# Optimization experiments

Hardware: AMD Instinct MI355X
Metric: run time of the kernel (lower is better)

Reference implementation:

```python
import jax, jax.numpy as jnp
import numpy as np


def _gcn(x, src, dst, W, b, n):
    # symmetric normalization: deg computed on edges WITH self-loops (weights 1)
    deg = jax.ops.segment_sum(jnp.ones_like(src, dtype=x.dtype), dst, num_segments=n)
    dinv = jnp.where(deg > 0, jax.lax.rsqrt(deg), 0.0)
    norm = dinv[src] * dinv[dst]              # [E+n]
    xw = x @ W                                # [n, out] transform first (cheaper)
    msg = xw[src] * norm[:, None]             # gather + edge scale
    return jax.ops.segment_sum(msg, dst, num_segments=n) + b


def setup_inputs() -> dict:
    key = jax.random.key(0)
    ks = jax.random.split(key, 8)
    N, E = 100_000, 1_280_000
    x = jax.random.normal(ks[0], (N, 18), dtype=jnp.float32)
    edge_index = jax.random.randint(ks[1], (2, E), 0, N, dtype=jnp.int32)
    W1 = jax.random.normal(ks[2], (18, 32), dtype=jnp.float32) * 0.2
    b1 = jnp.zeros((32,), dtype=jnp.float32)
    W2 = jax.random.normal(ks[3], (32, 64), dtype=jnp.float32) * 0.15
    b2 = jnp.zeros((64,), dtype=jnp.float32)
    Wfc = jax.random.normal(ks[4], (64, 2), dtype=jnp.float32) * 0.1
    bfc = jnp.zeros((2,), dtype=jnp.float32)
    return {"x": x, "edge_index": edge_index, "W1": W1, "b1": b1,
            "W2": W2, "b2": b2, "Wfc": Wfc, "bfc": bfc}


def reference(x, edge_index, W1, b1, W2, b2, Wfc, bfc):
    n = x.shape[0]
    loop = jnp.arange(n, dtype=edge_index.dtype)
    src = jnp.concatenate([edge_index[0], loop])   # add self-loops (PyG default)
    dst = jnp.concatenate([edge_index[1], loop])
    h = jax.nn.relu(_gcn(x, src, dst, W1, b1, n))
    h = jax.nn.relu(_gcn(h, src, dst, W2, b2, n))
    logits = h @ Wfc + bfc
    return jax.nn.log_softmax(logits, axis=1)
```

## Files before the change

kernel.cpp:

```cpp
#include <hip/hip_runtime.h>
#include <hip/hip_fp16.h>
#include <math.h>


#define TPB 256
#define BSH 8
#define BNODES 256
#define MAXBUCK 512
#define CH 4096
#define CAPSH 13
#define CAP (1 << CAPSH)

__global__ void k_part(const int* __restrict__ src, const int* __restrict__ dst,
                       int* __restrict__ bcursor, int* __restrict__ eb,
                       __half* __restrict__ u1h, __half* __restrict__ u2h,
                       int E, int n, int nbuck) {
    __shared__ int lh[MAXBUCK];
    __shared__ int lexc[MAXBUCK];
    __shared__ int lbase[MAXBUCK];
    __shared__ int sval[CH];
    __shared__ unsigned short sbk[CH];
    int t = threadIdx.x;
    if (blockIdx.x == 0 && t < 32) {
        u1h[(size_t)n * 32 + t] = __float2half_rn(0.f);
        u2h[(size_t)n * 32 + t] = __float2half_rn(0.f);
    }
    int chunk0 = blockIdx.x * CH;
    int end = min(chunk0 + CH, E);
    int cnt = end - chunk0;
    const int4* dst4 = (const int4*)dst;
    const int4* src4 = (const int4*)src;
    for (int i = t; i < MAXBUCK; i += TPB) lh[i] = 0;
    __syncthreads();
    for (int e4 = chunk0 / 4 + t; e4 * 4 < end; e4 += TPB) {
        int base = e4 * 4;
        int4 d = dst4[e4];
        if (base + 0 < end) atomicAdd(&lh[d.x >> BSH], 1);
        if (base + 1 < end) atomicAdd(&lh[d.y >> BSH], 1);
        if (base + 2 < end) atomicAdd(&lh[d.z >> BSH], 1);
        if (base + 3 < end) atomicAdd(&lh[d.w >> BSH], 1);
    }
    __syncthreads();
    for (int i = t; i < MAXBUCK; i += TPB) lexc[i] = lh[i];
    __syncthreads();
    for (int off = 1; off < MAXBUCK; off <<= 1) {
        int i1 = t + TPB;
        int v0 = (t >= off) ? lexc[t - off] : 0;
        int v1 = (i1 >= off) ? lexc[i1 - off] : 0;
        __syncthreads();
        lexc[t] += v0;
        lexc[i1] += v1;
        __syncthreads();
    }
    for (int i = t; i < MAXBUCK; i += TPB) {
        int c = lh[i];
        lbase[i] = c ? atomicAdd(&bcursor[i], c) : 0;
        lexc[i] -= c;
        lh[i] = 0;
    }
    __syncthreads();
    for (int e4 = chunk0 / 4 + t; e4 * 4 < end; e4 += TPB) {
        int base = e4 * 4;
        int4 d = dst4[e4];
        int4 s = src4[e4];
        #define PUTL(c, sv) if (base + c < end) { \
            int b = (d.sv) >> BSH; \
            int p = lexc[b] + atomicAdd(&lh[b], 1); \
            sval[p] = ((s.sv) << BSH) | ((d.sv) & (BNODES - 1)); \
            sbk[p] = (unsigned short)b; }
        PUTL(0, x) PUTL(1, y) PUTL(2, z) PUTL(3, w)
        #undef PUTL
    }
    __syncthreads();
    for (int i = t; i < cnt; i += TPB) {
        int b = sbk[i];
        int r = lbase[b] + (i - lexc[b]);
        if (r < CAP) eb[((size_t)b << CAPSH) + r] = sval[i];
    }
}

__global__ void k_bucket(const int* __restrict__ eb, const int* __restrict__ bcursor,
                         const float* __restrict__ x, const float* __restrict__ W1,
                         int* __restrict__ csr, int* __restrict__ row_start,
                         int* __restrict__ cnt8, float* __restrict__ dinv,
                         __half* __restrict__ u1h, int n) {
    __shared__ int lcnt[BNODES];
    __shared__ int lscan[BNODES];
    __shared__ float ldinv[BNODES];
    __shared__ float xs[BNODES * 18];
    int b = blockIdx.x;
    int t = threadIdx.x;
    int node0 = b << BSH;
    int beg = b << CAPSH;
    int end = beg + min(bcursor[b], CAP);
    lcnt[t] = 0;
    __syncthreads();
    for (int i = beg + t; i < end; i += TPB)
        atomicAdd(&lcnt[eb[i] & (BNODES - 1)], 1);
    __syncthreads();
    int v = lcnt[t];
    int pad = (v + 7) & ~7;
    lscan[t] = pad;
    __syncthreads();
    for (int off = 1; off < TPB; off <<= 1) {
        int xx = (t >= off) ? lscan[t - off] : 0;
        __syncthreads();
        lscan[t] += xx;
        __syncthreads();
    }
    int pexcl = lscan[t] - pad;
    int node = node0 + t;
    float dv = rsqrtf(1.0f + (float)v);
    ldinv[t] = dv;
    if (node < n) {
        row_start[node] = beg + pexcl;
        cnt8[node] = pad >> 3;
        dinv[node] = dv;
    }
    __syncthreads();
    lcnt[t] = pexcl;
    __syncthreads();
    for (int i = beg + t; i < end; i += TPB) {
        int e = eb[i];
        int p = atomicAdd(&lcnt[e & (BNODES - 1)], 1);
        csr[beg + p] = e >> BSH;
    }
    __syncthreads();
    for (int p = v; p < pad; ++p) csr[beg + pexcl + p] = n;
    int nn = min(BNODES, n - node0);
    const float* xb = x + (size_t)node0 * 18;
    int tot18 = nn * 18;
    for (int i = t; i < tot18; i += TPB) xs[i] = xb[i];
    __syncthreads();
    int f = t & 31, g = t >> 5;
    float w1r[18];
#pragma unroll
    for (int k = 0; k < 18; ++k) w1r[k] = W1[k * 32 + f];
    __half* ub = u1h + (size_t)node0 * 32;
    for (int nl = g; nl < nn; nl += 8) {
        const float* rp = &xs[nl * 18];
        float a = 0.f;
#pragma unroll
        for (int k = 0; k < 18; ++k) a = fmaf(rp[k], w1r[k], a);
        ub[nl * 32 + f] = __float2half_rn(a * ldinv[nl]);
    }
}

#define CVT4(vv, r0, r1, r2, r3) \
    { __half2* _p = (__half2*)&(vv); \
      float2 _fl = __half22float2(_p[0]), _fh = __half22float2(_p[1]); \
      r0 = _fl.x; r1 = _fl.y; r2 = _fh.x; r3 = _fh.y; }

#define GATHER8H(uq, sA, sB, q, a0, a1, a2, a3) \
    { uint2 _v0 = uq[(size_t)(sA).x * 8 + (q)]; \
      uint2 _v1 = uq[(size_t)(sA).y * 8 + (q)]; \
      uint2 _v2 = uq[(size_t)(sA).z * 8 + (q)]; \
      uint2 _v3 = uq[(size_t)(sA).w * 8 + (q)]; \
      uint2 _v4 = uq[(size_t)(sB).x * 8 + (q)]; \
      uint2 _v5 = uq[(size_t)(sB).y * 8 + (q)]; \
      uint2 _v6 = uq[(size_t)(sB).z * 8 + (q)]; \
      uint2 _v7 = uq[(size_t)(sB).w * 8 + (q)]; \
      __half2* _h0 = (__half2*)&_v0; __half2* _h1 = (__half2*)&_v1; \
      __half2* _h2 = (__half2*)&_v2; __half2* _h3 = (__half2*)&_v3; \
      __half2* _h4 = (__half2*)&_v4; __half2* _h5 = (__half2*)&_v5; \
      __half2* _h6 = (__half2*)&_v6; __half2* _h7 = (__half2*)&_v7; \
      __half2 _A01 = __hadd2(_h0[0], _h1[0]), _A23 = __hadd2(_h2[0], _h3[0]); \
      __half2 _A45 = __hadd2(_h4[0], _h5[0]), _A67 = __hadd2(_h6[0], _h7[0]); \
      __half2 _B01 = __hadd2(_h0[1], _h1[1]), _B23 = __hadd2(_h2[1], _h3[1]); \
      __half2 _B45 = __hadd2(_h4[1], _h5[1]), _B67 = __hadd2(_h6[1], _h7[1]); \
      __half2 _A03 = __hadd2(_A01, _A23), _A47 = __hadd2(_A45, _A67); \
      __half2 _B03 = __hadd2(_B01, _B23), _B47 = __hadd2(_B45, _B67); \
      float2 _fa0 = __half22float2(_A03), _fa1 = __half22float2(_A47); \
      float2 _fb0 = __half22float2(_B03), _fb1 = __half22float2(_B47); \
      a0 += _fa0.x + _fa1.x; \
      a1 += _fa0.y + _fa1.y; \
      a2 += _fb0.x + _fb1.x; \
      a3 += _fb0.y + _fb1.y; }

__global__ void k_fused1(const uint2* __restrict__ u1q, const int* __restrict__ row_start,
                         const int* __restrict__ cnt8, const int* __restrict__ csr,
                         const float* __restrict__ dinv,
                         const float* __restrict__ b1, __half* __restrict__ u2h,
                         int n) {
    int t = threadIdx.x;
    int lane = t & 63, wv = t >> 6;
    int q = lane & 7, grp = lane >> 3;
    int node = (blockIdx.x * 4 + wv) * 8 + grp;
    if (node >= n) return;
    float4 bb = ((const float4*)b1)[q];
    uint2 sv = u1q[(size_t)node * 8 + q];
    float a0, a1, a2, a3;
    CVT4(sv, a0, a1, a2, a3)
    int beg = row_start[node];
    int it = cnt8[node];
    const int4* ip = (const int4*)(csr + beg);
    if (it > 0) {
        int4 sA = ip[0], sB = ip[1];
        for (int i = 0; i < it; ++i) {
            int4 nA = ip[2 * i + 2];
            int4 nB = ip[2 * i + 3];
            GATHER8H(u1q, sA, sB, q, a0, a1, a2, a3)
            sA = nA; sB = nB;
        }
    }
    float di = dinv[node];
    float r0 = fmaxf(fmaf(di, a0, bb.x), 0.f) * di;
    float r1 = fmaxf(fmaf(di, a1, bb.y), 0.f) * di;
    float r2 = fmaxf(fmaf(di, a2, bb.z), 0.f) * di;
    float r3 = fmaxf(fmaf(di, a3, bb.w), 0.f) * di;
    uint2 st;
    __half2* sp = (__half2*)&st;
    sp[0].x = __float2half_rn(r0); sp[0].y = __float2half_rn(r1);
    sp[1].x = __float2half_rn(r2); sp[1].y = __float2half_rn(r3);
    ((uint2*)u2h)[(size_t)node * 8 + q] = st;
}

__global__ void k_fused2(const uint2* __restrict__ u2q, const int* __restrict__ row_start,
                         const int* __restrict__ cnt8, const int* __restrict__ csr,
                         const float* __restrict__ dinv,
                         const float* __restrict__ W2,
                         const float* __restrict__ b2, const float* __restrict__ Wfc,
                         const float* __restrict__ bfc, float* __restrict__ out,
                         int n) {
    __shared__ float lagg[4][8][33];
    int t = threadIdx.x;
    int lane = t & 63, wv = t >> 6;
    int q = lane & 7, grp = lane >> 3;
    float w2r[32];
#pragma unroll
    for (int k = 0; k < 32; ++k) w2r[k] = W2[k * 64 + lane];
    float b2v = b2[lane];
    float wf0 = Wfc[lane * 2 + 0], wf1 = Wfc[lane * 2 + 1];
    float bf0 = bfc[0], bf1 = bfc[1];
    int node0 = (blockIdx.x * 4 + wv) * 8;
    int node = node0 + grp;
    float a0 = 0.f, a1 = 0.f, a2 = 0.f, a3 = 0.f;
    if (node < n) {
        uint2 sv = u2q[(size_t)node * 8 + q];
        float s0, s1, s2, s3;
        CVT4(sv, s0, s1, s2, s3)
        a0 = s0; a1 = s1; a2 = s2; a3 = s3;
        int beg = row_start[node];
        int it = cnt8[node];
        const int4* ip = (const int4*)(csr + beg);
        if (it > 0) {
            int4 sA = ip[0], sB = ip[1];
            for (int i = 0; i < it; ++i) {
                int4 nA = ip[2 * i + 2];
                int4 nB = ip[2 * i + 3];
                GATHER8H(u2q, sA, sB, q, a0, a1, a2, a3)
                sA = nA; sB = nB;
            }
        }
    }
    lagg[wv][grp][4 * q + 0] = a0;
    lagg[wv][grp][4 * q + 1] = a1;
    lagg[wv][grp][4 * q + 2] = a2;
    lagg[wv][grp][4 * q + 3] = a3;
#pragma unroll
    for (int r = 0; r < 8; ++r) {
        int nodeT = node0 + r;
        const float* rp = lagg[wv][r];
        float c0 = 0.f, c1 = 0.f, c2 = 0.f, c3 = 0.f;
#pragma unroll
        for (int k = 0; k < 32; k += 4) {
            c0 = fmaf(rp[k],     w2r[k],     c0);
            c1 = fmaf(rp[k + 1], w2r[k + 1], c1);
            c2 = fmaf(rp[k + 2], w2r[k + 2], c2);
            c3 = fmaf(rp[k + 3], w2r[k + 3], c3);
        }
        float a = (c0 + c1) + (c2 + c3);
        float v = (nodeT < n) ? fmaxf(fmaf(dinv[nodeT], a, b2v), 0.f) : 0.f;
        float l0 = v * wf0;
        float l1 = v * wf1;
#pragma unroll
        for (int off = 32; off >= 1; off >>= 1) {
            l0 += __shfl_xor(l0, off, 64);
            l1 += __shfl_xor(l1, off, 64);
        }
        if (lane == 0 && nodeT < n) {
            l0 += bf0;
            l1 += bf1;
            float m2 = fmaxf(l0, l1);
            float lse = m2 + logf(expf(l0 - m2) + expf(l1 - m2));
            out[nodeT * 2 + 0] = l0 - lse;
            out[nodeT * 2 + 1] = l1 - lse;
        }
    }
}

extern "C" void kernel_launch(void* const* d_in, const int* in_sizes, int n_in,
                              void* d_out, int out_size, void* d_ws, size_t ws_size,
                              hipStream_t stream) {
    const float* x   = (const float*)d_in[0];
    const int*   ei  = (const int*)d_in[1];
    const float* W1  = (const float*)d_in[2];
    const float* b1  = (const float*)d_in[3];
    const float* W2  = (const float*)d_in[4];
    const float* b2  = (const float*)d_in[5];
    const float* Wfc = (const float*)d_in[6];
    const float* bfc = (const float*)d_in[7];
    float* out = (float*)d_out;

    const int n = in_sizes[0] / 18;
    const int E = in_sizes[1] / 2;
    const int* src = ei;
    const int* dst = ei + E;
    const int nbuck = (n + BNODES - 1) >> BSH;

    char* w = (char*)d_ws;
    int*    bcursor   = (int*)w;     w += (size_t)nbuck * 4;
    int*    row_start = (int*)w;     w += (size_t)n * 4;
    int*    cnt8      = (int*)w;     w += (size_t)n * 4;
    float*  dinv      = (float*)w;   w += (size_t)n * 4;
    int*    eb        = (int*)w;     w += (size_t)nbuck * CAP * 4;
    int*    csr       = (int*)w;     w += (size_t)nbuck * CAP * 4 + 64;
    w = (char*)(((size_t)w + 63) & ~(size_t)63);
    __half* u1h       = (__half*)w;  w += (size_t)(n + 1) * 32 * 2;
    w = (char*)(((size_t)w + 63) & ~(size_t)63);
    __half* u2h       = (__half*)w;  w += (size_t)(n + 1) * 32 * 2;

    hipMemsetAsync(bcursor, 0, (size_t)nbuck * 4, stream);
    k_part<<<(E + CH - 1) / CH, TPB, 0, stream>>>(src, dst, bcursor, eb, u1h, u2h, E, n, nbuck);
    k_bucket<<<nbuck, TPB, 0, stream>>>(eb, bcursor, x, W1, csr, row_start, cnt8,
                                        dinv, u1h, n);

    const int waves = (n + 7) / 8;
    const int blocksF = (waves + 3) / 4;

    k_fused1<<<blocksF, TPB, 0, stream>>>((const uint2*)u1h, row_start, cnt8, csr,
                                          dinv, b1, u2h, n);
    k_fused2<<<blocksF, TPB, 0, stream>>>((const uint2*)u2h, row_start, cnt8, csr,
                                          dinv, W2, b2, Wfc, bfc, out, n);
}
```

Baseline: 170.1 us.

## Replace two-pass bucket partition with global degree count and atomic CSR scatter

```diff
diff --git a/kernel.cpp b/kernel.cpp
--- a/kernel.cpp
+++ b/kernel.cpp
@@ -6,85 +6,32 @@
 #define TPB 256
 #define BSH 8
 #define BNODES 256
-#define MAXBUCK 512
-#define CH 4096
 #define CAPSH 13
 #define CAP (1 << CAPSH)
 
-__global__ void k_part(const int* __restrict__ src, const int* __restrict__ dst,
-                       int* __restrict__ bcursor, int* __restrict__ eb,
-                       __half* __restrict__ u1h, __half* __restrict__ u2h,
-                       int E, int n, int nbuck) {
-    __shared__ int lh[MAXBUCK];
-    __shared__ int lexc[MAXBUCK];
-    __shared__ int lbase[MAXBUCK];
-    __shared__ int sval[CH];
-    __shared__ unsigned short sbk[CH];
+__global__ void k_deg(const int* __restrict__ dst, int* __restrict__ deg,
+                      __half* __restrict__ u1h, __half* __restrict__ u2h,
+                      int E4, int E, int n) {
     int t = threadIdx.x;
     if (blockIdx.x == 0 && t < 32) {
         u1h[(size_t)n * 32 + t] = __float2half_rn(0.f);
         u2h[(size_t)n * 32 + t] = __float2half_rn(0.f);
     }
-    int chunk0 = blockIdx.x * CH;
-    int end = min(chunk0 + CH, E);
-    int cnt = end - chunk0;
-    const int4* dst4 = (const int4*)dst;
-    const int4* src4 = (const int4*)src;
-    for (int i = t; i < MAXBUCK; i += TPB) lh[i] = 0;
-    __syncthreads();
-    for (int e4 = chunk0 / 4 + t; e4 * 4 < end; e4 += TPB) {
-        int base = e4 * 4;
-        int4 d = dst4[e4];
-        if (base + 0 < end) atomicAdd(&lh[d.x >> BSH], 1);
-        if (base + 1 < end) atomicAdd(&lh[d.y >> BSH], 1);
-        if (base + 2 < end) atomicAdd(&lh[d.z >> BSH], 1);
-        if (base + 3 < end) atomicAdd(&lh[d.w >> BSH], 1);
-    }
-    __syncthreads();
-    for (int i = t; i < MAXBUCK; i += TPB) lexc[i] = lh[i];
-    __syncthreads();
-    for (int off = 1; off < MAXBUCK; off <<= 1) {
-        int i1 = t + TPB;
-        int v0 = (t >= off) ? lexc[t - off] : 0;
-        int v1 = (i1 >= off) ? lexc[i1 - off] : 0;
-        __syncthreads();
-        lexc[t] += v0;
-        lexc[i1] += v1;
-        __syncthreads();
-    }
-    for (int i = t; i < MAXBUCK; i += TPB) {
-        int c = lh[i];
-        lbase[i] = c ? atomicAdd(&bcursor[i], c) : 0;
-        lexc[i] -= c;
-        lh[i] = 0;
-    }
-    __syncthreads();
-    for (int e4 = chunk0 / 4 + t; e4 * 4 < end; e4 += TPB) {
-        int base = e4 * 4;
-        int4 d = dst4[e4];
-        int4 s = src4[e4];
-        #define PUTL(c, sv) if (base + c < end) { \
-            int b = (d.sv) >> BSH; \
-            int p = lexc[b] + atomicAdd(&lh[b], 1); \
-            sval[p] = ((s.sv) << BSH) | ((d.sv) & (BNODES - 1)); \
-            sbk[p] = (unsigned short)b; }
-        PUTL(0, x) PUTL(1, y) PUTL(2, z) PUTL(3, w)
-        #undef PUTL
-    }
-    __syncthreads();
-    for (int i = t; i < cnt; i += TPB) {
-        int b = sbk[i];
-        int r = lbase[b] + (i - lexc[b]);
-        if (r < CAP) eb[((size_t)b << CAPSH) + r] = sval[i];
-    }
-}
-
-__global__ void k_bucket(const int* __restrict__ eb, const int* __restrict__ bcursor,
-                         const float* __restrict__ x, const float* __restrict__ W1,
-                         int* __restrict__ csr, int* __restrict__ row_start,
-                         int* __restrict__ cnt8, float* __restrict__ dinv,
-                         __half* __restrict__ u1h, int n) {
-    __shared__ int lcnt[BNODES];
+    int i = blockIdx.x * TPB + t;
+    if (i >= E4) return;
+    int4 d = ((const int4*)dst)[i];
+    int base = i * 4;
+    atomicAdd(&deg[d.x], 1);
+    if (base + 1 < E) atomicAdd(&deg[d.y], 1);
+    if (base + 2 < E) atomicAdd(&deg[d.z], 1);
+    if (base + 3 < E) atomicAdd(&deg[d.w], 1);
+}
+
+__global__ void k_bucket2(const int* __restrict__ deg, const float* __restrict__ x,
+                          const float* __restrict__ W1,
+                          int* __restrict__ csr, int* __restrict__ row_start,
+                          int* __restrict__ cnt8, float* __restrict__ dinv,
+                          __half* __restrict__ u1h, int n) {
     __shared__ int lscan[BNODES];
     __shared__ float ldinv[BNODES];
     __shared__ float xs[BNODES * 18];
@@ -92,13 +39,8 @@
     int t = threadIdx.x;
     int node0 = b << BSH;
     int beg = b << CAPSH;
-    int end = beg + min(bcursor[b], CAP);
-    lcnt[t] = 0;
-    __syncthreads();
-    for (int i = beg + t; i < end; i += TPB)
-        atomicAdd(&lcnt[eb[i] & (BNODES - 1)], 1);
-    __syncthreads();
-    int v = lcnt[t];
+    int node = node0 + t;
+    int v = (node < n) ? deg[node] : 0;
     int pad = (v + 7) & ~7;
     lscan[t] = pad;
     __syncthreads();
@@ -109,7 +51,6 @@
         __syncthreads();
     }
     int pexcl = lscan[t] - pad;
-    int node = node0 + t;
     float dv = rsqrtf(1.0f + (float)v);
     ldinv[t] = dv;
     if (node < n) {
@@ -117,15 +58,6 @@
         cnt8[node] = pad >> 3;
         dinv[node] = dv;
     }
-    __syncthreads();
-    lcnt[t] = pexcl;
-    __syncthreads();
-    for (int i = beg + t; i < end; i += TPB) {
-        int e = eb[i];
-        int p = atomicAdd(&lcnt[e & (BNODES - 1)], 1);
-        csr[beg + p] = e >> BSH;
-    }
-    __syncthreads();
     for (int p = v; p < pad; ++p) csr[beg + pexcl + p] = n;
     int nn = min(BNODES, n - node0);
     const float* xb = x + (size_t)node0 * 18;
@@ -144,6 +76,22 @@
         for (int k = 0; k < 18; ++k) a = fmaf(rp[k], w1r[k], a);
         ub[nl * 32 + f] = __float2half_rn(a * ldinv[nl]);
     }
+}
+
+__global__ void k_scatter(const int* __restrict__ src, const int* __restrict__ dst,
+                          const int* __restrict__ row_start, int* __restrict__ cursor,
+                          int* __restrict__ csr, int E4, int E) {
+    int i = blockIdx.x * TPB + threadIdx.x;
+    if (i >= E4) return;
+    int4 d = ((const int4*)dst)[i];
+    int4 s = ((const int4*)src)[i];
+    int base = i * 4;
+    #define SC(c, sv) if (base + c < E) { \
+        int dd = d.sv; \
+        int r = atomicAdd(&cursor[dd], 1); \
+        csr[row_start[dd] + r] = s.sv; }
+    SC(0, x) SC(1, y) SC(2, z) SC(3, w)
+    #undef SC
 }
 
 #define CVT4(vv, r0, r1, r2, r3) \
@@ -309,21 +257,24 @@
     const int nbuck = (n + BNODES - 1) >> BSH;
 
     char* w = (char*)d_ws;
-    int*    bcursor   = (int*)w;     w += (size_t)nbuck * 4;
+    int*    deg       = (int*)w;     w += (size_t)n * 4;
+    int*    cursor    = (int*)w;     w += (size_t)n * 4;
     int*    row_start = (int*)w;     w += (size_t)n * 4;
     int*    cnt8      = (int*)w;     w += (size_t)n * 4;
     float*  dinv      = (float*)w;   w += (size_t)n * 4;
-    int*    eb        = (int*)w;     w += (size_t)nbuck * CAP * 4;
     int*    csr       = (int*)w;     w += (size_t)nbuck * CAP * 4 + 64;
     w = (char*)(((size_t)w + 63) & ~(size_t)63);
     __half* u1h       = (__half*)w;  w += (size_t)(n + 1) * 32 * 2;
     w = (char*)(((size_t)w + 63) & ~(size_t)63);
     __half* u2h       = (__half*)w;  w += (size_t)(n + 1) * 32 * 2;
 
-    hipMemsetAsync(bcursor, 0, (size_t)nbuck * 4, stream);
-    k_part<<<(E + CH - 1) / CH, TPB, 0, stream>>>(src, dst, bcursor, eb, u1h, u2h, E, n, nbuck);
-    k_bucket<<<nbuck, TPB, 0, stream>>>(eb, bcursor, x, W1, csr, row_start, cnt8,
-                                        dinv, u1h, n);
+    hipMemsetAsync(deg, 0, (size_t)2 * n * 4, stream);
+    const int E4 = (E + 3) / 4;
+    const int edgeBlocks = (E4 + TPB - 1) / TPB;
+    k_deg<<<edgeBlocks, TPB, 0, stream>>>(dst, deg, u1h, u2h, E4, E, n);
+    k_bucket2<<<nbuck, TPB, 0, stream>>>(deg, x, W1, csr, row_start, cnt8,
+                                         dinv, u1h, n);
+    k_scatter<<<edgeBlocks, TPB, 0, stream>>>(src, dst, row_start, cursor, csr, E4, E);
 
     const int waves = (n + 7) / 8;
     const int blocksF = (waves + 3) / 4;
```

Result: slower. 281.8 us (+65.6%).
